# Optimization experiments

Measured on AMD Instinct MI355X. Metric: run time of the kernel, lower is better.

## Reference

```python
import jax, jax.numpy as jnp
import numpy as np

EMBED = 1024
HEADS = 16
DIM_HEAD = EMBED // HEADS
N, L = 4, 2048


def setup_inputs() -> dict:
    key = jax.random.key(0)
    ks = jax.random.split(key, 12)
    s = 0.02
    return {
        "q": jax.random.normal(ks[0], (N, L, EMBED), jnp.float32),
        "k": jax.random.normal(ks[1], (N, L, EMBED), jnp.float32),
        "v": jax.random.normal(ks[2], (N, L, EMBED), jnp.float32),
        "padding_mask": jnp.ones((N, L), dtype=bool),
        "sequence_mask": jnp.zeros((L, L), dtype=bool),
        # Linear(in, out): store weight as [out, in] like torch, bias [out]
        "Wq": jax.random.normal(ks[3], (EMBED, EMBED), jnp.float32) * s,
        "bq": jnp.zeros((EMBED,), jnp.float32),
        "Wk": jax.random.normal(ks[4], (EMBED, EMBED), jnp.float32) * s,
        "bk": jnp.zeros((EMBED,), jnp.float32),
        "Wv": jax.random.normal(ks[5], (EMBED, EMBED), jnp.float32) * s,
        "bv": jnp.zeros((EMBED,), jnp.float32),
        "Wo": jax.random.normal(ks[6], (EMBED, EMBED), jnp.float32) * s,
        "bo": jnp.zeros((EMBED,), jnp.float32),
    }


def reference(q, k, v, padding_mask, sequence_mask, Wq, bq, Wk, bk, Wv, bv, Wo, bo):
    n, lq, _ = q.shape
    lk = k.shape[1]
    # input projections
    qp = (q @ Wq.T + bq).reshape(n, lq, HEADS, DIM_HEAD)
    kp = (k @ Wk.T + bk).reshape(n, lk, HEADS, DIM_HEAD)
    vp = (v @ Wv.T + bv).reshape(n, lk, HEADS, DIM_HEAD)
    # energy: [n, h, lq, lk]
    energy = jnp.einsum('nqhd,nkhd->nhqk', qp, kp)
    attention = jax.nn.softmax(energy / jnp.sqrt(jnp.float32(EMBED)), axis=3)
    # NOTE: the original torch code calls masked_fill (non in-place) and
    # discards the result, so padding_mask / sequence_mask have NO effect.
    # Dropout is also never applied in forward. Replicated faithfully.
    out = jnp.einsum('nhqk,nkhd->nqhd', attention, vp)
    out = out.reshape(n, lq, EMBED)
    return out @ Wo.T + bo
```

## Files before the change

### kernel.cpp

```cpp
#include <hip/hip_runtime.h>
#include <stdint.h>

typedef _Float16 f16;
typedef _Float16 f16x8 __attribute__((ext_vector_type(8)));
typedef _Float16 f16x4 __attribute__((ext_vector_type(4)));
typedef _Float16 f16x2 __attribute__((ext_vector_type(2)));
typedef float f32x4 __attribute__((ext_vector_type(4)));

__device__ __forceinline__ f32x4 mfma16(f16x8 a, f16x8 b, f32x4 c) {
    return __builtin_amdgcn_mfma_f32_16x16x32_f16(a, b, c, 0, 0, 0);
}

__device__ __forceinline__ void gload16(const f16* g, f16* l) {
    __builtin_amdgcn_global_load_lds(
        (const __attribute__((address_space(1))) uint32_t*)g,
        (__attribute__((address_space(3))) uint32_t*)l, 16, 0, 0);
}

template <bool OUT16>
__device__ __forceinline__ void gemm_body(const f16* __restrict__ A,
                                          const f16* __restrict__ B,
                                          const float* __restrict__ bias,
                                          void* __restrict__ Cout, long ldo,
                                          int biasrow, float scale,
                                          long m0, long n0, f16* As, f16* Bs) {
    int tid = threadIdx.x;
    int lane = tid & 63, w = tid >> 6;
    int wm = w & 1, wn = w >> 1;
    int l15 = lane & 15, quad = lane >> 4;

    int rg = lane >> 3;
    int cg = (lane & 7) ^ rg;
    const f16* ag[4];
    const f16* bg[4];
    f16* al[4];
    f16* bl[4];
#pragma unroll
    for (int t = 0; t < 4; ++t) {
        int rb = (w * 4 + t) * 8;
        ag[t] = A + (m0 + rb + rg) * 1024 + cg * 8;
        bg[t] = B + (n0 + rb + rg) * 1024 + cg * 8;
        al[t] = &As[rb * 64];
        bl[t] = &Bs[rb * 64];
    }

    f32x4 acc[4][4] = {};

    for (int k0 = 0; k0 < 1024; k0 += 64) {
        __syncthreads();
#pragma unroll
        for (int t = 0; t < 4; ++t) {
            gload16(ag[t] + k0, al[t]);
            gload16(bg[t] + k0, bl[t]);
        }
        __syncthreads();
#pragma unroll
        for (int ks = 0; ks < 2; ++ks) {
            int cc = (ks * 4 + quad) ^ (l15 & 7);
            f16x8 af[4], bf[4];
#pragma unroll
            for (int t = 0; t < 4; ++t) {
                af[t] = *(const f16x8*)&As[(wm * 64 + t * 16 + l15) * 64 + cc * 8];
                bf[t] = *(const f16x8*)&Bs[(wn * 64 + t * 16 + l15) * 64 + cc * 8];
            }
#pragma unroll
            for (int i = 0; i < 4; ++i)
#pragma unroll
                for (int j = 0; j < 4; ++j)
                    acc[i][j] = mfma16(af[i], bf[j], acc[i][j]);
        }
    }

#pragma unroll
    for (int i = 0; i < 4; ++i) {
        int mrow = wm * 64 + i * 16 + quad * 4;
#pragma unroll
        for (int j = 0; j < 4; ++j) {
            int ncol = wn * 64 + j * 16 + l15;
            long gn = n0 + ncol;
#pragma unroll
            for (int r = 0; r < 4; ++r) {
                long gm = m0 + mrow + r;
                float v = (acc[i][j][r] + (biasrow ? bias[gm] : bias[gn])) * scale;
                if constexpr (OUT16)
                    ((f16*)Cout)[gm * ldo + gn] = (f16)v;
                else
                    ((float*)Cout)[gm * ldo + gn] = v;
            }
        }
    }
}

__global__ __launch_bounds__(256, 2) void qkv_proj(
    const f16* __restrict__ qh, const f16* __restrict__ kh,
    const f16* __restrict__ vh, const f16* __restrict__ Wh,
    const float* __restrict__ bq, const float* __restrict__ bk,
    const float* __restrict__ bv, f16* __restrict__ Qp, f16* __restrict__ Kp,
    f16* __restrict__ Vt) {
    __shared__ __align__(16) f16 As[128 * 64];
    __shared__ __align__(16) f16 Bs[128 * 64];
    int z = blockIdx.z;
    const f16* A;
    const f16* B;
    const float* bias;
    f16* C;
    long ldo;
    int biasrow;
    float scale;
    if (z == 0) {
        A = qh; B = Wh; bias = bq; C = Qp; ldo = 1024; biasrow = 0;
        scale = 0.0450842200277786f;
    } else if (z == 1) {
        A = kh; B = Wh + 1048576; bias = bk; C = Kp; ldo = 1024; biasrow = 0;
        scale = 1.0f;
    } else {
        A = Wh + 2097152; B = vh; bias = bv; C = Vt; ldo = 8192; biasrow = 1;
        scale = 1.0f;
    }
    long m0 = (long)(z == 2 ? blockIdx.y : blockIdx.x) * 128;
    long n0 = (long)(z == 2 ? blockIdx.x : blockIdx.y) * 128;
    gemm_body<true>(A, B, bias, C, ldo, biasrow, scale, m0, n0, As, Bs);
}

__global__ __launch_bounds__(256, 2) void o_proj(const f16* __restrict__ Op,
                                                 const f16* __restrict__ Wo,
                                                 const float* __restrict__ bo,
                                                 float* __restrict__ out) {
    __shared__ __align__(16) f16 As[128 * 64];
    __shared__ __align__(16) f16 Bs[128 * 64];
    gemm_body<false>(Op, Wo, bo, out, 1024, 0, 1.0f, (long)blockIdx.x * 128,
                     (long)blockIdx.y * 128, As, Bs);
}

__global__ __launch_bounds__(256, 3) void attn128(const f16* __restrict__ Qp,
                                                  const f16* __restrict__ Kp,
                                                  const f16* __restrict__ Vt,
                                                  f16* __restrict__ Op) {
    __shared__ __align__(16) f16 QPs[128 * 64];
    __shared__ __align__(16) f16 Ks[2][64 * 64];
    __shared__ __align__(16) f16 Vs[2][64 * 64];
    __shared__ float lsi[128];

    int tid = threadIdx.x;
    int lane = tid & 63, w = tid >> 6;
    int l15 = lane & 15, quad = lane >> 4;
    int b = blockIdx.x;
    int xcd = b & 7, slot = b >> 3;
    int nh = xcd * 8 + (slot >> 4);
    int qt = slot & 15;
    int nb = nh >> 4, h = nh & 15;
    long tok0 = (long)nb * 2048;

    int rg = lane >> 3, cg = (lane & 7) ^ rg;

    const f16* qsrc = Qp + (tok0 + qt * 128) * 1024 + h * 64;
#pragma unroll
    for (int t = 0; t < 4; ++t) {
        int rb = w * 32 + t * 8;
        gload16(qsrc + (rb + rg) * 1024 + cg * 8, &QPs[rb * 64]);
    }
    const f16* kptr = Kp + (tok0 + w * 16 + rg) * 1024 + h * 64 + cg * 8;
    const f16* vptr = Vt + ((long)h * 64 + w * 16 + rg) * 8192 + tok0 + cg * 8;
    gload16(kptr, &Ks[0][(w * 16) * 64]);
    gload16(kptr + 8 * 1024, &Ks[0][(w * 16 + 8) * 64]);
    gload16(vptr, &Vs[0][(w * 16) * 64]);
    gload16(vptr + (long)8 * 8192, &Vs[0][(w * 16 + 8) * 64]);
    const f16* kn = kptr + 65536;
    const f16* vn = vptr + 64;
    __syncthreads();

    f16x8 qf[2][2];
#pragma unroll
    for (int ks = 0; ks < 2; ++ks) {
        int cc = (ks * 4 + quad) ^ (l15 & 7);
#pragma unroll
        for (int j = 0; j < 2; ++j)
            qf[ks][j] = *(const f16x8*)&QPs[(w * 32 + j * 16 + l15) * 64 + cc * 8];
    }

    f32x4 oacc[2][4] = {};
    float rsum[2] = {0.f, 0.f};
    const f32x4 z4 = {0.f, 0.f, 0.f, 0.f};

    for (int kt = 0; kt < 32; ++kt) {
        int cur = kt & 1;
        f32x4 sacc[4][2];
        {
            int cc0 = quad ^ (l15 & 7);
            int cc1 = (4 + quad) ^ (l15 & 7);
            f16x8 a0[4], a1[4];
#pragma unroll
            for (int t = 0; t < 4; ++t) {
                a0[t] = *(const f16x8*)&Ks[cur][(t * 16 + l15) * 64 + cc0 * 8];
                a1[t] = *(const f16x8*)&Ks[cur][(t * 16 + l15) * 64 + cc1 * 8];
            }
#pragma unroll
            for (int i = 0; i < 4; ++i)
#pragma unroll
                for (int j = 0; j < 2; ++j) {
                    sacc[i][j] = mfma16(a0[i], qf[0][j], z4);
                    sacc[i][j] = mfma16(a1[i], qf[1][j], sacc[i][j]);
                }
        }
        if (kt < 31) {
            int nxt = cur ^ 1;
            f16* kd = &Ks[nxt][(w * 16) * 64];
            f16* vd = &Vs[nxt][(w * 16) * 64];
            gload16(kn, kd);
            gload16(kn + 8 * 1024, kd + 8 * 64);
            gload16(vn, vd);
            gload16(vn + (long)8 * 8192, vd + 8 * 64);
            kn += 65536;
            vn += 64;
        }
#pragma unroll
        for (int i = 0; i < 4; ++i) {
#pragma unroll
            for (int j = 0; j < 2; ++j) {
                float p0 = __builtin_amdgcn_exp2f(sacc[i][j][0]);
                float p1 = __builtin_amdgcn_exp2f(sacc[i][j][1]);
                float p2 = __builtin_amdgcn_exp2f(sacc[i][j][2]);
                float p3 = __builtin_amdgcn_exp2f(sacc[i][j][3]);
                rsum[j] += (p0 + p1) + (p2 + p3);
                f16x2 lo = __builtin_bit_cast(f16x2, __builtin_amdgcn_cvt_pkrtz(p0, p1));
                f16x2 hi = __builtin_bit_cast(f16x2, __builtin_amdgcn_cvt_pkrtz(p2, p3));
                f16x4 ph;
                ph[0] = lo[0]; ph[1] = lo[1]; ph[2] = hi[0]; ph[3] = hi[1];
                int qrow = w * 32 + j * 16 + l15;
                int kl = i * 16 + quad * 4;
                int c = kl >> 3;
                *(f16x4*)&QPs[qrow * 64 + ((c ^ (qrow & 7)) << 3) + (kl & 7)] = ph;
            }
        }
#pragma unroll
        for (int ks = 0; ks < 2; ++ks) {
            int cc = (ks * 4 + quad) ^ (l15 & 7);
            f16x8 af[2], bf[4];
#pragma unroll
            for (int i = 0; i < 2; ++i)
                af[i] = *(const f16x8*)&QPs[(w * 32 + i * 16 + l15) * 64 + cc * 8];
#pragma unroll
            for (int j = 0; j < 4; ++j)
                bf[j] = *(const f16x8*)&Vs[cur][(j * 16 + l15) * 64 + cc * 8];
#pragma unroll
            for (int i = 0; i < 2; ++i)
#pragma unroll
                for (int j = 0; j < 4; ++j)
                    oacc[i][j] = mfma16(af[i], bf[j], oacc[i][j]);
        }
        __syncthreads();
    }

#pragma unroll
    for (int j = 0; j < 2; ++j) {
        rsum[j] += __shfl_xor(rsum[j], 16, 64);
        rsum[j] += __shfl_xor(rsum[j], 32, 64);
    }
    if (lane < 16) {
        lsi[w * 32 + lane] = 1.0f / rsum[0];
        lsi[w * 32 + 16 + lane] = 1.0f / rsum[1];
    }

    long otok = tok0 + (long)qt * 128;
#pragma unroll
    for (int i = 0; i < 2; ++i) {
        int qrow = w * 32 + i * 16 + quad * 4;
#pragma unroll
        for (int j = 0; j < 4; ++j) {
            int d = j * 16 + l15;
#pragma unroll
            for (int r = 0; r < 4; ++r) {
                float v = oacc[i][j][r] * lsi[qrow + r];
                Op[(otok + qrow + r) * 1024 + h * 64 + d] = (f16)v;
            }
        }
    }
}

__global__ void cvt_all(const float* __restrict__ q, const float* __restrict__ k,
                        const float* __restrict__ v, const float* __restrict__ w0,
                        const float* __restrict__ w1, const float* __restrict__ w2,
                        const float* __restrict__ w3, f16* __restrict__ qh,
                        f16* __restrict__ kh, f16* __restrict__ vh,
                        f16* __restrict__ wh) {
    long id = (long)blockIdx.x * 256 + threadIdx.x;
    const float* s;
    f16* d;
    long off;
    if (id < 3145728) {
        int which = (int)(id >> 20);
        off = (id & 1048575) * 8;
        s = which == 0 ? q : which == 1 ? k : v;
        d = which == 0 ? qh : which == 1 ? kh : vh;
    } else {
        long id2 = id - 3145728;
        int wi = (int)(id2 >> 17);
        off = (id2 & 131071) * 8;
        s = wi == 0 ? w0 : wi == 1 ? w1 : wi == 2 ? w2 : w3;
        d = wh + (long)wi * 1048576;
    }
    f32x4 a = *(const f32x4*)(s + off);
    f32x4 b = *(const f32x4*)(s + off + 4);
    f16x8 hv;
    hv[0] = (f16)a[0]; hv[1] = (f16)a[1]; hv[2] = (f16)a[2]; hv[3] = (f16)a[3];
    hv[4] = (f16)b[0]; hv[5] = (f16)b[1]; hv[6] = (f16)b[2]; hv[7] = (f16)b[3];
    *(f16x8*)(d + off) = hv;
}

extern "C" void kernel_launch(void* const* d_in, const int* in_sizes, int n_in,
                              void* d_out, int out_size, void* d_ws, size_t ws_size,
                              hipStream_t stream) {
    const float* q  = (const float*)d_in[0];
    const float* k  = (const float*)d_in[1];
    const float* v  = (const float*)d_in[2];
    const float* Wq = (const float*)d_in[5];
    const float* bq = (const float*)d_in[6];
    const float* Wk = (const float*)d_in[7];
    const float* bk = (const float*)d_in[8];
    const float* Wv = (const float*)d_in[9];
    const float* bv = (const float*)d_in[10];
    const float* Wo = (const float*)d_in[11];
    const float* bo = (const float*)d_in[12];

    char* ws = (char*)d_ws;
    f16* qh = (f16*)ws;
    f16* kh = (f16*)(ws + (16L << 20));
    f16* vh = (f16*)(ws + (32L << 20));
    f16* Wh = (f16*)(ws + (48L << 20));
    f16* Qp = (f16*)(ws + (56L << 20));
    f16* Kp = (f16*)(ws + (72L << 20));
    f16* Vt = (f16*)(ws + (88L << 20));
    f16* Op = (f16*)(ws + (104L << 20));

    cvt_all<<<14336, 256, 0, stream>>>(q, k, v, Wq, Wk, Wv, Wo, qh, kh, vh, Wh);

    qkv_proj<<<dim3(64, 8, 3), 256, 0, stream>>>(qh, kh, vh, Wh, bq, bk, bv,
                                                 Qp, Kp, Vt);

    attn128<<<1024, 256, 0, stream>>>(Qp, Kp, Vt, Op);

    o_proj<<<dim3(64, 8), 256, 0, stream>>>(Op, Wh + 3145728, bo, (float*)d_out);
}
```

Before: 331.0 us.

## Process two query tiles per attention block to share K/V tile loads

The attention kernel now handles 256 query rows per block as two 128-row halves. Each K/V tile and its LDS fragments are loaded once and fed to both halves, which halves global K/V traffic and LDS fragment reads per query row. The grid shrinks from 1024 to 512 blocks, and the occupancy hint drops from 3 to 2 blocks per SM. The price is doubled accumulator registers and more LDS per block, which could cause spilling or hurt latency hiding.

Measured after the change: 321.4 us. 1.03x faster.

```diff
diff --git a/kernel.cpp b/kernel.cpp
--- a/kernel.cpp
+++ b/kernel.cpp
@@ -132,32 +132,35 @@
                      (long)blockIdx.y * 128, As, Bs);
 }
 
-__global__ __launch_bounds__(256, 3) void attn128(const f16* __restrict__ Qp,
+__global__ __launch_bounds__(256, 2) void attn256(const f16* __restrict__ Qp,
                                                   const f16* __restrict__ Kp,
                                                   const f16* __restrict__ Vt,
                                                   f16* __restrict__ Op) {
-    __shared__ __align__(16) f16 QPs[128 * 64];
+    __shared__ __align__(16) f16 Ps0[128 * 64];
+    __shared__ __align__(16) f16 Ps1[128 * 64];
     __shared__ __align__(16) f16 Ks[2][64 * 64];
     __shared__ __align__(16) f16 Vs[2][64 * 64];
-    __shared__ float lsi[128];
 
     int tid = threadIdx.x;
     int lane = tid & 63, w = tid >> 6;
     int l15 = lane & 15, quad = lane >> 4;
     int b = blockIdx.x;
     int xcd = b & 7, slot = b >> 3;
-    int nh = xcd * 8 + (slot >> 4);
-    int qt = slot & 15;
+    int nh = xcd * 8 + (slot >> 3);
+    int qp = slot & 7;
     int nb = nh >> 4, h = nh & 15;
     long tok0 = (long)nb * 2048;
+    long qrow0 = qp * 256;
 
     int rg = lane >> 3, cg = (lane & 7) ^ rg;
 
-    const f16* qsrc = Qp + (tok0 + qt * 128) * 1024 + h * 64;
+    const f16* qsrc0 = Qp + (tok0 + qrow0) * 1024 + h * 64;
+    const f16* qsrc1 = qsrc0 + 128 * 1024;
 #pragma unroll
     for (int t = 0; t < 4; ++t) {
         int rb = w * 32 + t * 8;
-        gload16(qsrc + (rb + rg) * 1024 + cg * 8, &QPs[rb * 64]);
+        gload16(qsrc0 + (rb + rg) * 1024 + cg * 8, &Ps0[rb * 64]);
+        gload16(qsrc1 + (rb + rg) * 1024 + cg * 8, &Ps1[rb * 64]);
     }
     const f16* kptr = Kp + (tok0 + w * 16 + rg) * 1024 + h * 64 + cg * 8;
     const f16* vptr = Vt + ((long)h * 64 + w * 16 + rg) * 8192 + tok0 + cg * 8;
@@ -169,37 +172,42 @@
     const f16* vn = vptr + 64;
     __syncthreads();
 
-    f16x8 qf[2][2];
+    f16x8 qf0[2][2], qf1[2][2];
 #pragma unroll
     for (int ks = 0; ks < 2; ++ks) {
         int cc = (ks * 4 + quad) ^ (l15 & 7);
 #pragma unroll
-        for (int j = 0; j < 2; ++j)
-            qf[ks][j] = *(const f16x8*)&QPs[(w * 32 + j * 16 + l15) * 64 + cc * 8];
-    }
-
-    f32x4 oacc[2][4] = {};
-    float rsum[2] = {0.f, 0.f};
+        for (int j = 0; j < 2; ++j) {
+            qf0[ks][j] = *(const f16x8*)&Ps0[(w * 32 + j * 16 + l15) * 64 + cc * 8];
+            qf1[ks][j] = *(const f16x8*)&Ps1[(w * 32 + j * 16 + l15) * 64 + cc * 8];
+        }
+    }
+
+    f32x4 oacc0[2][4] = {}, oacc1[2][4] = {};
+    float rs0[2] = {0.f, 0.f}, rs1[2] = {0.f, 0.f};
     const f32x4 z4 = {0.f, 0.f, 0.f, 0.f};
 
     for (int kt = 0; kt < 32; ++kt) {
         int cur = kt & 1;
-        f32x4 sacc[4][2];
-        {
-            int cc0 = quad ^ (l15 & 7);
-            int cc1 = (4 + quad) ^ (l15 & 7);
-            f16x8 a0[4], a1[4];
-#pragma unroll
-            for (int t = 0; t < 4; ++t) {
-                a0[t] = *(const f16x8*)&Ks[cur][(t * 16 + l15) * 64 + cc0 * 8];
-                a1[t] = *(const f16x8*)&Ks[cur][(t * 16 + l15) * 64 + cc1 * 8];
-            }
+        f32x4 sacc0[4][2], sacc1[4][2];
+#pragma unroll
+        for (int ks = 0; ks < 2; ++ks) {
+            int cc = (ks * 4 + quad) ^ (l15 & 7);
+            f16x8 a[4];
+#pragma unroll
+            for (int t = 0; t < 4; ++t)
+                a[t] = *(const f16x8*)&Ks[cur][(t * 16 + l15) * 64 + cc * 8];
 #pragma unroll
             for (int i = 0; i < 4; ++i)
 #pragma unroll
                 for (int j = 0; j < 2; ++j) {
-                    sacc[i][j] = mfma16(a0[i], qf[0][j], z4);
-                    sacc[i][j] = mfma16(a1[i], qf[1][j], sacc[i][j]);
+                    if (ks == 0) {
+                        sacc0[i][j] = mfma16(a[i], qf0[0][j], z4);
+                        sacc1[i][j] = mfma16(a[i], qf1[0][j], z4);
+                    } else {
+                        sacc0[i][j] = mfma16(a[i], qf0[1][j], sacc0[i][j]);
+                        sacc1[i][j] = mfma16(a[i], qf1[1][j], sacc1[i][j]);
+                    }
                 }
         }
         if (kt < 31) {
@@ -217,51 +225,76 @@
         for (int i = 0; i < 4; ++i) {
 #pragma unroll
             for (int j = 0; j < 2; ++j) {
-                float p0 = __builtin_amdgcn_exp2f(sacc[i][j][0]);
-                float p1 = __builtin_amdgcn_exp2f(sacc[i][j][1]);
-                float p2 = __builtin_amdgcn_exp2f(sacc[i][j][2]);
-                float p3 = __builtin_amdgcn_exp2f(sacc[i][j][3]);
-                rsum[j] += (p0 + p1) + (p2 + p3);
-                f16x2 lo = __builtin_bit_cast(f16x2, __builtin_amdgcn_cvt_pkrtz(p0, p1));
-                f16x2 hi = __builtin_bit_cast(f16x2, __builtin_amdgcn_cvt_pkrtz(p2, p3));
-                f16x4 ph;
-                ph[0] = lo[0]; ph[1] = lo[1]; ph[2] = hi[0]; ph[3] = hi[1];
                 int qrow = w * 32 + j * 16 + l15;
                 int kl = i * 16 + quad * 4;
                 int c = kl >> 3;
-                *(f16x4*)&QPs[qrow * 64 + ((c ^ (qrow & 7)) << 3) + (kl & 7)] = ph;
+                int off = qrow * 64 + ((c ^ (qrow & 7)) << 3) + (kl & 7);
+                {
+                    float p0 = __builtin_amdgcn_exp2f(sacc0[i][j][0]);
+                    float p1 = __builtin_amdgcn_exp2f(sacc0[i][j][1]);
+                    float p2 = __builtin_amdgcn_exp2f(sacc0[i][j][2]);
+                    float p3 = __builtin_amdgcn_exp2f(sacc0[i][j][3]);
+                    rs0[j] += (p0 + p1) + (p2 + p3);
+                    f16x2 lo = __builtin_bit_cast(f16x2, __builtin_amdgcn_cvt_pkrtz(p0, p1));
+                    f16x2 hi = __builtin_bit_cast(f16x2, __builtin_amdgcn_cvt_pkrtz(p2, p3));
+                    f16x4 ph;
+                    ph[0] = lo[0]; ph[1] = lo[1]; ph[2] = hi[0]; ph[3] = hi[1];
+                    *(f16x4*)&Ps0[off] = ph;
+                }
+                {
+                    float p0 = __builtin_amdgcn_exp2f(sacc1[i][j][0]);
+                    float p1 = __builtin_amdgcn_exp2f(sacc1[i][j][1]);
+                    float p2 = __builtin_amdgcn_exp2f(sacc1[i][j][2]);
+                    float p3 = __builtin_amdgcn_exp2f(sacc1[i][j][3]);
+                    rs1[j] += (p0 + p1) + (p2 + p3);
+                    f16x2 lo = __builtin_bit_cast(f16x2, __builtin_amdgcn_cvt_pkrtz(p0, p1));
+                    f16x2 hi = __builtin_bit_cast(f16x2, __builtin_amdgcn_cvt_pkrtz(p2, p3));
+                    f16x4 ph;
+                    ph[0] = lo[0]; ph[1] = lo[1]; ph[2] = hi[0]; ph[3] = hi[1];
+                    *(f16x4*)&Ps1[off] = ph;
+                }
             }
         }
 #pragma unroll
         for (int ks = 0; ks < 2; ++ks) {
             int cc = (ks * 4 + quad) ^ (l15 & 7);
-            f16x8 af[2], bf[4];
-#pragma unroll
-            for (int i = 0; i < 2; ++i)
-                af[i] = *(const f16x8*)&QPs[(w * 32 + i * 16 + l15) * 64 + cc * 8];
+            f16x8 bf[4];
 #pragma unroll
             for (int j = 0; j < 4; ++j)
                 bf[j] = *(const f16x8*)&Vs[cur][(j * 16 + l15) * 64 + cc * 8];
+            f16x8 af0[2], af1[2];
+#pragma unroll
+            for (int i = 0; i < 2; ++i) {
+                af0[i] = *(const f16x8*)&Ps0[(w * 32 + i * 16 + l15) * 64 + cc * 8];
+                af1[i] = *(const f16x8*)&Ps1[(w * 32 + i * 16 + l15) * 64 + cc * 8];
+            }
 #pragma unroll
             for (int i = 0; i < 2; ++i)
 #pragma unroll
-                for (int j = 0; j < 4; ++j)
-                    oacc[i][j] = mfma16(af[i], bf[j], oacc[i][j]);
+                for (int j = 0; j < 4; ++j) {
+                    oacc0[i][j] = mfma16(af0[i], bf[j], oacc0[i][j]);
+                    oacc1[i][j] = mfma16(af1[i], bf[j], oacc1[i][j]);
+                }
         }
         __syncthreads();
     }
 
+    float* lsi = (float*)&Ks[0][0];
 #pragma unroll
     for (int j = 0; j < 2; ++j) {
-        rsum[j] += __shfl_xor(rsum[j], 16, 64);
-        rsum[j] += __shfl_xor(rsum[j], 32, 64);
+        rs0[j] += __shfl_xor(rs0[j], 16, 64);
+        rs0[j] += __shfl_xor(rs0[j], 32, 64);
+        rs1[j] += __shfl_xor(rs1[j], 16, 64);
+        rs1[j] += __shfl_xor(rs1[j], 32, 64);
     }
     if (lane < 16) {
-        lsi[w * 32 + lane] = 1.0f / rsum[0];
-        lsi[w * 32 + 16 + lane] = 1.0f / rsum[1];
-    }
-
-    long otok = tok0 + (long)qt * 128;
+        lsi[w * 32 + lane] = 1.0f / rs0[0];
+        lsi[w * 32 + 16 + lane] = 1.0f / rs0[1];
+        lsi[128 + w * 32 + lane] = 1.0f / rs1[0];
+        lsi[128 + w * 32 + 16 + lane] = 1.0f / rs1[1];
+    }
+
+    long otok = tok0 + qrow0;
 #pragma unroll
     for (int i = 0; i < 2; ++i) {
         int qrow = w * 32 + i * 16 + quad * 4;
@@ -270,8 +303,10 @@
             int d = j * 16 + l15;
 #pragma unroll
             for (int r = 0; r < 4; ++r) {
-                float v = oacc[i][j][r] * lsi[qrow + r];
-                Op[(otok + qrow + r) * 1024 + h * 64 + d] = (f16)v;
+                Op[(otok + qrow + r) * 1024 + h * 64 + d] =
+                    (f16)(oacc0[i][j][r] * lsi[qrow + r]);
+                Op[(otok + 128 + qrow + r) * 1024 + h * 64 + d] =
+                    (f16)(oacc1[i][j][r] * lsi[128 + qrow + r]);
             }
         }
     }
@@ -337,7 +372,7 @@
     qkv_proj<<<dim3(64, 8, 3), 256, 0, stream>>>(qh, kh, vh, Wh, bq, bk, bv,
                                                  Qp, Kp, Vt);
 
-    attn128<<<1024, 256, 0, stream>>>(Qp, Kp, Vt, Op);
+    attn256<<<512, 256, 0, stream>>>(Qp, Kp, Vt, Op);
 
     o_proj<<<dim3(64, 8), 256, 0, stream>>>(Op, Wh + 3145728, bo, (float*)d_out);
 }
```
